# Kernel tuning notes

Hardware: AMD Instinct MI355X
Metric: run time of the kernel (lower is better)

Reference implementation:

```python
import jax, jax.numpy as jnp
import numpy as np

NUM_QUANTIZERS = 4  # num_quantizers


def setup_inputs() -> dict:
    key = jax.random.key(0)
    k1, k2 = jax.random.split(key)
    x = jax.random.normal(k1, (8, 64, 128, 128), dtype=jnp.float32)
    codebook = jax.random.normal(k2, (512, 64), dtype=jnp.float32)
    return {"x": x, "codebook": codebook}


def reference(x, codebook):
    """Residual VQ with shared Euclidean codebook, straight-through estimator.

    x: [B, C, H, W] image feature map; codebook: [K, C].
    Returns (quantized [B,C,H,W], indices [B,H,W,Q] int32, commit_loss [Q]).
    """
    B, C, H, W = x.shape
    flat = x.transpose(0, 2, 3, 1).reshape(-1, C)  # [N, C], N = B*H*W
    c_sq = jnp.sum(codebook * codebook, axis=-1)   # [K]

    residual = flat
    quant_out = jnp.zeros_like(flat)
    idx_list, losses = [], []
    for _ in range(NUM_QUANTIZERS):
        # argmin ||r - c||^2 == argmin (||c||^2 - 2 r.c); ||r||^2 constant per row
        dist = c_sq[None, :] - 2.0 * (residual @ codebook.T)  # [N, K]
        idx = jnp.argmin(dist, axis=-1)                        # [N]
        quant = codebook[idx]                                  # [N, C] gather
        # commitment loss: mse(stop_grad(quant), residual)
        losses.append(jnp.mean(jnp.square(jax.lax.stop_gradient(quant) - residual)))
        # straight-through: gradients flow to residual, not codebook
        quant_st = residual + jax.lax.stop_gradient(quant - residual)
        quant_out = quant_out + quant_st
        residual = residual - jax.lax.stop_gradient(quant)
        idx_list.append(idx)

    quantized = quant_out.reshape(B, H, W, C).transpose(0, 3, 1, 2)
    indices = jnp.stack(idx_list, axis=-1).reshape(B, H, W, NUM_QUANTIZERS)
    commit_loss = jnp.stack(losses)
    return quantized, indices, commit_loss
```

## Files before the change

kernel.cpp:

```cpp
#include <hip/hip_runtime.h>


#define NPTS   131072
#define CH     64
#define KCODE  512
#define NQ     4
#define HW     16384
#define BPTS   64
#define BTHR   256
#define CCH    8
#define NCHK   8

__device__ __forceinline__ void load_lds16(const float* g, float* l) {
    __builtin_amdgcn_global_load_lds(
        (const __attribute__((address_space(1))) void*)g,
        (__attribute__((address_space(3))) void*)l, 16, 0, 0);
}

__global__ void prep_cbS(const float* __restrict__ cb, float* __restrict__ cbS) {
    int g = blockIdx.x * 256 + threadIdx.x;
    int c = g >> 9, pos = g & 511;
    int i = pos >> 7, cg = (pos >> 2) & 31, j = pos & 3;
    int k = cg * 16 + i * 4 + j;
    cbS[g] = cb[k * CH + c];
}

__global__ void prep_csq(const float* __restrict__ cb, float* __restrict__ csq) {
    int k = blockIdx.x * 256 + threadIdx.x;
    if (k < KCODE) {
        const float4* row = (const float4*)(cb + (size_t)k * CH);
        float a0 = 0.f, a1 = 0.f, a2 = 0.f, a3 = 0.f;
#pragma unroll
        for (int j = 0; j < CH / 4; ++j) {
            float4 v = row[j];
            a0 = fmaf(v.x, v.x, a0); a1 = fmaf(v.y, v.y, a1);
            a2 = fmaf(v.z, v.z, a2); a3 = fmaf(v.w, v.w, a3);
        }
        csq[k] = (a0 + a1) + (a2 + a3);
    }
}

__global__ __launch_bounds__(BTHR, 3) void rvq_main(
    const float* __restrict__ x, const float* __restrict__ cb,
    const float* __restrict__ cbS, const float* __restrict__ csq_g,
    float* __restrict__ out_quant, float* __restrict__ out_idx,
    float* __restrict__ out_loss)
{
    __shared__ __align__(16) float s_res[CH * BPTS];
    __shared__ __align__(16) float s_buf[2][CCH * KCODE];
    __shared__ __align__(16) float s_csq[KCODE];
    __shared__ int   s_bidx[BPTS];
    __shared__ int   s_idx4[BPTS * NQ];
    __shared__ float s_ls[4 * BPTS];

    const int tid  = threadIdx.x;
    const int lane = tid & 63;
    const int w    = tid >> 6;
    const int cg   = tid & 31;
    const int pg   = tid >> 5;

    const int n0  = blockIdx.x * BPTS;
    const int b   = n0 >> 14;
    const int hw0 = n0 & (HW - 1);
    const float* xbase = x + (size_t)b * CH * HW + hw0;

#pragma unroll
    for (int r = 0; r < 4; ++r) {
        int off = (w * 4 + r) * 256;
        load_lds16(cbS + off + lane * 4, &s_buf[0][off]);
    }

    for (int j = tid; j < CH * BPTS / 4; j += BTHR) {
        int c = j >> 4, p4 = j & 15;
        *(float4*)&s_res[c * BPTS + p4 * 4] =
            *(const float4*)(xbase + (size_t)c * HW + p4 * 4);
    }
    for (int j = tid; j < KCODE; j += BTHR) s_csq[j] = csq_g[j];
    __syncthreads();

    float lossq[NQ], idxf[NQ];

    for (int q = 0; q < NQ; ++q) {
        float acc[8][16];
        {
            const float4* cq4 = (const float4*)(s_csq + cg * 16);
            float4 c0 = cq4[0], c1 = cq4[1], c2 = cq4[2], c3 = cq4[3];
            float ci[16] = {c0.x, c0.y, c0.z, c0.w, c1.x, c1.y, c1.z, c1.w,
                            c2.x, c2.y, c2.z, c2.w, c3.x, c3.y, c3.z, c3.w};
#pragma unroll
            for (int p = 0; p < 8; ++p)
#pragma unroll
                for (int n = 0; n < 16; ++n) acc[p][n] = -0.5f * ci[n];
        }

        for (int chk = 0; chk < NCHK; ++chk) {
            if (!(q == NQ - 1 && chk == NCHK - 1)) {
                const int nchk = (chk + 1 < NCHK) ? chk + 1 : 0;
                const float* src = cbS + nchk * (CCH * KCODE);
                float* dst = s_buf[(chk + 1) & 1];
#pragma unroll
                for (int r = 0; r < 4; ++r) {
                    int off = (w * 4 + r) * 256;
                    load_lds16(src + off + lane * 4, dst + off);
                }
            }

            const float* bufp = s_buf[chk & 1];
#pragma unroll 2
            for (int c = 0; c < CCH; ++c) {
                const float* ar = &s_res[(chk * CCH + c) * BPTS + pg * 8];
                float4 a0 = *(const float4*)(ar + 0);
                float4 a1 = *(const float4*)(ar + 4);
                float av[8] = {a0.x, a0.y, a0.z, a0.w, a1.x, a1.y, a1.z, a1.w};
                const float* br = &bufp[c * KCODE + cg * 4];
#pragma unroll
                for (int nb = 0; nb < 4; ++nb) {
                    float4 bq = *(const float4*)(br + nb * 128);
#pragma unroll
                    for (int p = 0; p < 8; ++p) {
                        acc[p][nb * 4 + 0] = fmaf(av[p], bq.x, acc[p][nb * 4 + 0]);
                        acc[p][nb * 4 + 1] = fmaf(av[p], bq.y, acc[p][nb * 4 + 1]);
                        acc[p][nb * 4 + 2] = fmaf(av[p], bq.z, acc[p][nb * 4 + 2]);
                        acc[p][nb * 4 + 3] = fmaf(av[p], bq.w, acc[p][nb * 4 + 3]);
                    }
                }
            }
            __syncthreads();
        }

        float bd[8]; int bi[8];
#pragma unroll
        for (int p = 0; p < 8; ++p) {
            float B = acc[p][0]; int I = cg * 16;
#pragma unroll
            for (int n = 1; n < 16; ++n)
                if (acc[p][n] > B) { B = acc[p][n]; I = cg * 16 + n; }
            bd[p] = B; bi[p] = I;
        }

#pragma unroll
        for (int m = 1; m <= 16; m <<= 1) {
#pragma unroll
            for (int p = 0; p < 8; ++p) {
                float oB = __shfl_xor(bd[p], m, 64);
                int   oI = __shfl_xor(bi[p], m, 64);
                if (oB > bd[p] || (oB == bd[p] && oI < bi[p])) {
                    bd[p] = oB; bi[p] = oI;
                }
            }
        }
        if (cg == 0) {
#pragma unroll
            for (int p = 0; p < 8; ++p) {
                s_bidx[pg * 8 + p] = bi[p];
                s_idx4[(pg * 8 + p) * 4 + q] = bi[p];
            }
        }
        __syncthreads();
        if (tid < BPTS) idxf[q] = (float)s_bidx[tid];

        {
            const int p  = tid & 63;
            const int cq = tid >> 6;
            int bix = s_bidx[p];
            const float4* crow = (const float4*)(cb + (size_t)bix * CH + cq * 16);
            float l0 = 0.f, l1 = 0.f, l2 = 0.f, l3 = 0.f;
#pragma unroll
            for (int i = 0; i < 4; ++i) {
                float4 v = crow[i];
                int c = cq * 16 + i * 4;
                float r0 = s_res[(c + 0) * BPTS + p] - v.x;
                float r1 = s_res[(c + 1) * BPTS + p] - v.y;
                float r2 = s_res[(c + 2) * BPTS + p] - v.z;
                float r3 = s_res[(c + 3) * BPTS + p] - v.w;
                s_res[(c + 0) * BPTS + p] = r0;
                s_res[(c + 1) * BPTS + p] = r1;
                s_res[(c + 2) * BPTS + p] = r2;
                s_res[(c + 3) * BPTS + p] = r3;
                l0 = fmaf(r0, r0, l0); l1 = fmaf(r1, r1, l1);
                l2 = fmaf(r2, r2, l2); l3 = fmaf(r3, r3, l3);
            }
            s_ls[cq * BPTS + p] = (l0 + l1) + (l2 + l3);
        }
        __syncthreads();
        if (tid < BPTS)
            lossq[q] = (s_ls[0 * BPTS + tid] + s_ls[1 * BPTS + tid]) +
                       (s_ls[2 * BPTS + tid] + s_ls[3 * BPTS + tid]);
    }

    {
        const int p  = tid & 63;
        const int cq = tid >> 6;
        int e0 = s_idx4[p * 4 + 0], e1 = s_idx4[p * 4 + 1];
        int e2 = s_idx4[p * 4 + 2], e3 = s_idx4[p * 4 + 3];
        const float4* r0 = (const float4*)(cb + (size_t)e0 * CH + cq * 16);
        const float4* r1 = (const float4*)(cb + (size_t)e1 * CH + cq * 16);
        const float4* r2 = (const float4*)(cb + (size_t)e2 * CH + cq * 16);
        const float4* r3 = (const float4*)(cb + (size_t)e3 * CH + cq * 16);
        float* ob = out_quant + (size_t)b * CH * HW + hw0;
#pragma unroll
        for (int i = 0; i < 4; ++i) {
            float4 v0 = r0[i], v1 = r1[i], v2 = r2[i], v3 = r3[i];
            float s0 = ((v0.x + v1.x) + v2.x) + v3.x;
            float s1 = ((v0.y + v1.y) + v2.y) + v3.y;
            float s2 = ((v0.z + v1.z) + v2.z) + v3.z;
            float s3 = ((v0.w + v1.w) + v2.w) + v3.w;
            int c = cq * 16 + i * 4;
            ob[(size_t)(c + 0) * HW + p] = s0;
            ob[(size_t)(c + 1) * HW + p] = s1;
            ob[(size_t)(c + 2) * HW + p] = s2;
            ob[(size_t)(c + 3) * HW + p] = s3;
        }
    }

    if (tid < BPTS) {
        ((float4*)out_idx)[n0 + tid] =
            make_float4(idxf[0], idxf[1], idxf[2], idxf[3]);
#pragma unroll
        for (int qq = 0; qq < NQ; ++qq) {
            float v = lossq[qq];
            for (int off = 32; off > 0; off >>= 1) v += __shfl_down(v, off, 64);
            if (tid == 0)
                atomicAdd(&out_loss[qq], v * (1.0f / 8388608.0f));
        }
    }
}

extern "C" void kernel_launch(void* const* d_in, const int* in_sizes, int n_in,
                              void* d_out, int out_size, void* d_ws, size_t ws_size,
                              hipStream_t stream) {
    const float* x  = (const float*)d_in[0];
    const float* cb = (const float*)d_in[1];
    float* out       = (float*)d_out;
    float* out_quant = out;
    float* out_idx   = out + 8388608;
    float* out_loss  = out + 8388608 + 524288;

    float* cbS = (float*)d_ws;
    float* csq = cbS + CH * KCODE;

    hipMemsetAsync(out_loss, 0, NQ * sizeof(float), stream);
    prep_cbS<<<(CH * KCODE) / 256, 256, 0, stream>>>(cb, cbS);
    prep_csq<<<2, 256, 0, stream>>>(cb, csq);
    rvq_main<<<NPTS / BPTS, BTHR, 0, stream>>>(x, cb, cbS, csq,
                                               out_quant, out_idx, out_loss);
}
```

Baseline: 521.1 us.

## Update residual scores via codebook Gram matrix with exact fallback for near ties

```diff
diff --git a/kernel.cpp b/kernel.cpp
--- a/kernel.cpp
+++ b/kernel.cpp
@@ -10,6 +10,7 @@
 #define BTHR   256
 #define CCH    8
 #define NCHK   8
+#define TAU    1.0e-2f
 
 __device__ __forceinline__ void load_lds16(const float* g, float* l) {
     __builtin_amdgcn_global_load_lds(
@@ -40,9 +41,29 @@
     }
 }
 
-__global__ __launch_bounds__(BTHR, 3) void rvq_main(
+__global__ void prep_gram(const float* __restrict__ cb, float* __restrict__ G) {
+    __shared__ float srow[CH];
+    const int kb = blockIdx.x;
+    if (threadIdx.x < CH / 4)
+        ((float4*)srow)[threadIdx.x] =
+            ((const float4*)(cb + (size_t)kb * CH))[threadIdx.x];
+    __syncthreads();
+#pragma unroll
+    for (int r = 0; r < 2; ++r) {
+        int k = threadIdx.x + r * 256;
+        const float* row = cb + (size_t)k * CH;
+        double a = 0.0;
+        for (int j = 0; j < CH; ++j) a += (double)srow[j] * (double)row[j];
+        G[(size_t)kb * KCODE + k] = (float)a;
+    }
+}
+
+__global__ __launch_bounds__(BTHR)
+__attribute__((amdgpu_waves_per_eu(3, 3)))
+void rvq_main(
     const float* __restrict__ x, const float* __restrict__ cb,
     const float* __restrict__ cbS, const float* __restrict__ csq_g,
+    const float* __restrict__ G,
     float* __restrict__ out_quant, float* __restrict__ out_idx,
     float* __restrict__ out_loss)
 {
@@ -52,6 +73,9 @@
     __shared__ int   s_bidx[BPTS];
     __shared__ int   s_idx4[BPTS * NQ];
     __shared__ float s_ls[4 * BPTS];
+    __shared__ unsigned int s_mask[2];
+    __shared__ float s_rwB[4];
+    __shared__ int   s_rwI[4];
 
     const int tid  = threadIdx.x;
     const int lane = tid & 63;
@@ -69,7 +93,6 @@
         int off = (w * 4 + r) * 256;
         load_lds16(cbS + off + lane * 4, &s_buf[0][off]);
     }
-
     for (int j = tid; j < CH * BPTS / 4; j += BTHR) {
         int c = j >> 4, p4 = j & 15;
         *(float4*)&s_res[c * BPTS + p4 * 4] =
@@ -80,83 +103,186 @@
 
     float lossq[NQ], idxf[NQ];
 
-    for (int q = 0; q < NQ; ++q) {
-        float acc[8][16];
-        {
-            const float4* cq4 = (const float4*)(s_csq + cg * 16);
-            float4 c0 = cq4[0], c1 = cq4[1], c2 = cq4[2], c3 = cq4[3];
-            float ci[16] = {c0.x, c0.y, c0.z, c0.w, c1.x, c1.y, c1.z, c1.w,
-                            c2.x, c2.y, c2.z, c2.w, c3.x, c3.y, c3.z, c3.w};
-#pragma unroll
-            for (int p = 0; p < 8; ++p)
-#pragma unroll
-                for (int n = 0; n < 16; ++n) acc[p][n] = -0.5f * ci[n];
-        }
-
-        for (int chk = 0; chk < NCHK; ++chk) {
-            if (!(q == NQ - 1 && chk == NCHK - 1)) {
-                const int nchk = (chk + 1 < NCHK) ? chk + 1 : 0;
-                const float* src = cbS + nchk * (CCH * KCODE);
-                float* dst = s_buf[(chk + 1) & 1];
-#pragma unroll
-                for (int r = 0; r < 4; ++r) {
-                    int off = (w * 4 + r) * 256;
-                    load_lds16(src + off + lane * 4, dst + off);
+    float acc[8][16];
+    {
+        const float4* cq4 = (const float4*)(s_csq + cg * 16);
+        float4 c0 = cq4[0], c1 = cq4[1], c2 = cq4[2], c3 = cq4[3];
+        float ci[16] = {c0.x, c0.y, c0.z, c0.w, c1.x, c1.y, c1.z, c1.w,
+                        c2.x, c2.y, c2.z, c2.w, c3.x, c3.y, c3.z, c3.w};
+#pragma unroll
+        for (int p = 0; p < 8; ++p)
+#pragma unroll
+            for (int n = 0; n < 16; ++n) acc[p][n] = -0.5f * ci[n];
+    }
+
+    for (int chk = 0; chk < NCHK; ++chk) {
+        if (chk < NCHK - 1) {
+            const float* src = cbS + (chk + 1) * (CCH * KCODE);
+            float* dst = s_buf[(chk + 1) & 1];
+#pragma unroll
+            for (int r = 0; r < 4; ++r) {
+                int off = (w * 4 + r) * 256;
+                load_lds16(src + off + lane * 4, dst + off);
+            }
+        }
+        const float* bufp = s_buf[chk & 1];
+#pragma unroll 2
+        for (int c = 0; c < CCH; ++c) {
+            const float* ar = &s_res[(chk * CCH + c) * BPTS + pg * 8];
+            float4 a0 = *(const float4*)(ar + 0);
+            float4 a1 = *(const float4*)(ar + 4);
+            float av[8] = {a0.x, a0.y, a0.z, a0.w, a1.x, a1.y, a1.z, a1.w};
+            const float* br = &bufp[c * KCODE + cg * 4];
+#pragma unroll
+            for (int nb = 0; nb < 4; ++nb) {
+                float4 bq = *(const float4*)(br + nb * 128);
+#pragma unroll
+                for (int p = 0; p < 8; ++p) {
+                    acc[p][nb * 4 + 0] = fmaf(av[p], bq.x, acc[p][nb * 4 + 0]);
+                    acc[p][nb * 4 + 1] = fmaf(av[p], bq.y, acc[p][nb * 4 + 1]);
+                    acc[p][nb * 4 + 2] = fmaf(av[p], bq.z, acc[p][nb * 4 + 2]);
+                    acc[p][nb * 4 + 3] = fmaf(av[p], bq.w, acc[p][nb * 4 + 3]);
                 }
             }
-
-            const float* bufp = s_buf[chk & 1];
-#pragma unroll 2
-            for (int c = 0; c < CCH; ++c) {
-                const float* ar = &s_res[(chk * CCH + c) * BPTS + pg * 8];
-                float4 a0 = *(const float4*)(ar + 0);
-                float4 a1 = *(const float4*)(ar + 4);
-                float av[8] = {a0.x, a0.y, a0.z, a0.w, a1.x, a1.y, a1.z, a1.w};
-                const float* br = &bufp[c * KCODE + cg * 4];
-#pragma unroll
-                for (int nb = 0; nb < 4; ++nb) {
-                    float4 bq = *(const float4*)(br + nb * 128);
-#pragma unroll
-                    for (int p = 0; p < 8; ++p) {
-                        acc[p][nb * 4 + 0] = fmaf(av[p], bq.x, acc[p][nb * 4 + 0]);
-                        acc[p][nb * 4 + 1] = fmaf(av[p], bq.y, acc[p][nb * 4 + 1]);
-                        acc[p][nb * 4 + 2] = fmaf(av[p], bq.z, acc[p][nb * 4 + 2]);
-                        acc[p][nb * 4 + 3] = fmaf(av[p], bq.w, acc[p][nb * 4 + 3]);
-                    }
+        }
+        __syncthreads();
+    }
+
+#pragma unroll
+    for (int p = 0; p < 8; ++p) {
+        float B = acc[p][0]; int I = cg * 16;
+#pragma unroll
+        for (int n = 1; n < 16; ++n)
+            if (acc[p][n] > B) { B = acc[p][n]; I = cg * 16 + n; }
+#pragma unroll
+        for (int m = 1; m <= 16; m <<= 1) {
+            float oB = __shfl_xor(B, m, 64);
+            int   oI = __shfl_xor(I, m, 64);
+            if (oB > B || (oB == B && oI < I)) { B = oB; I = oI; }
+        }
+        if (cg == 0) {
+            s_bidx[pg * 8 + p] = I;
+            s_idx4[(pg * 8 + p) * 4 + 0] = I;
+        }
+    }
+    __syncthreads();
+    if (tid < BPTS) idxf[0] = (float)s_bidx[tid];
+
+    {
+        const int p  = tid & 63;
+        const int cq = tid >> 6;
+        int bix = s_bidx[p];
+        const float4* crow = (const float4*)(cb + (size_t)bix * CH + cq * 16);
+        float l0 = 0.f, l1 = 0.f, l2 = 0.f, l3 = 0.f;
+#pragma unroll
+        for (int i = 0; i < 4; ++i) {
+            float4 v = crow[i];
+            int c = cq * 16 + i * 4;
+            float r0 = s_res[(c + 0) * BPTS + p] - v.x;
+            float r1 = s_res[(c + 1) * BPTS + p] - v.y;
+            float r2 = s_res[(c + 2) * BPTS + p] - v.z;
+            float r3 = s_res[(c + 3) * BPTS + p] - v.w;
+            s_res[(c + 0) * BPTS + p] = r0;
+            s_res[(c + 1) * BPTS + p] = r1;
+            s_res[(c + 2) * BPTS + p] = r2;
+            s_res[(c + 3) * BPTS + p] = r3;
+            l0 = fmaf(r0, r0, l0); l1 = fmaf(r1, r1, l1);
+            l2 = fmaf(r2, r2, l2); l3 = fmaf(r3, r3, l3);
+        }
+        s_ls[cq * BPTS + p] = (l0 + l1) + (l2 + l3);
+    }
+    __syncthreads();
+    if (tid < BPTS)
+        lossq[0] = (s_ls[0 * BPTS + tid] + s_ls[1 * BPTS + tid]) +
+                   (s_ls[2 * BPTS + tid] + s_ls[3 * BPTS + tid]);
+
+    for (int q = 1; q < NQ; ++q) {
+        int bix8[8];
+#pragma unroll
+        for (int p = 0; p < 8; ++p) bix8[p] = s_bidx[pg * 8 + p];
+        if (tid < 2) s_mask[tid] = 0;
+        __syncthreads();
+
+#pragma unroll
+        for (int p = 0; p < 8; ++p) {
+            const float4* grow =
+                (const float4*)(G + (size_t)bix8[p] * KCODE + cg * 16);
+#pragma unroll
+            for (int nb = 0; nb < 4; ++nb) {
+                float4 g = grow[nb];
+                acc[p][nb * 4 + 0] -= g.x;
+                acc[p][nb * 4 + 1] -= g.y;
+                acc[p][nb * 4 + 2] -= g.z;
+                acc[p][nb * 4 + 3] -= g.w;
+            }
+            float B = acc[p][0]; int I = cg * 16; float B2 = -3.4e38f;
+#pragma unroll
+            for (int n = 1; n < 16; ++n) {
+                float v = acc[p][n];
+                if (v > B)      { B2 = B; B = v; I = cg * 16 + n; }
+                else if (v > B2) B2 = v;
+            }
+#pragma unroll
+            for (int m = 1; m <= 16; m <<= 1) {
+                float oB  = __shfl_xor(B, m, 64);
+                int   oI  = __shfl_xor(I, m, 64);
+                float oB2 = __shfl_xor(B2, m, 64);
+                float nB2;
+                if (oB > B)       { nB2 = fmaxf(B, oB2); B = oB; I = oI; }
+                else if (oB == B) { nB2 = fmaxf(B2, oB2); if (oI < I) I = oI; }
+                else              { nB2 = fmaxf(B2, oB); }
+                B2 = nB2;
+            }
+            if (cg == 0) {
+                s_bidx[pg * 8 + p] = I;
+                s_idx4[(pg * 8 + p) * 4 + q] = I;
+                if (B - B2 < TAU)
+                    atomicOr(&s_mask[(pg * 8 + p) >> 5],
+                             1u << ((pg * 8 + p) & 31));
+            }
+        }
+        __syncthreads();
+
+        unsigned long long mask =
+            (unsigned long long)s_mask[0] |
+            ((unsigned long long)s_mask[1] << 32);
+        while (mask) {
+            int p = (int)__builtin_ctzll(mask);
+            mask &= mask - 1;
+            float Bb = -3.4e38f; int Ib = 0;
+#pragma unroll
+            for (int rr = 0; rr < 2; ++rr) {
+                int k = tid + rr * 256;
+                const float4* crow = (const float4*)(cb + (size_t)k * CH);
+                float d0 = 0.f, d1 = 0.f, d2 = 0.f, d3 = 0.f;
+#pragma unroll
+                for (int j = 0; j < 16; ++j) {
+                    float4 v = crow[j];
+                    d0 = fmaf(v.x, s_res[(j * 4 + 0) * BPTS + p], d0);
+                    d1 = fmaf(v.y, s_res[(j * 4 + 1) * BPTS + p], d1);
+                    d2 = fmaf(v.z, s_res[(j * 4 + 2) * BPTS + p], d2);
+                    d3 = fmaf(v.w, s_res[(j * 4 + 3) * BPTS + p], d3);
                 }
-            }
+                float s = fmaf(-0.5f, s_csq[k], (d0 + d1) + (d2 + d3));
+                if (s > Bb) { Bb = s; Ib = k; }
+            }
+#pragma unroll
+            for (int m = 1; m <= 32; m <<= 1) {
+                float oB = __shfl_xor(Bb, m, 64);
+                int   oI = __shfl_xor(Ib, m, 64);
+                if (oB > Bb || (oB == Bb && oI < Ib)) { Bb = oB; Ib = oI; }
+            }
+            if (lane == 0) { s_rwB[w] = Bb; s_rwI[w] = Ib; }
             __syncthreads();
-        }
-
-        float bd[8]; int bi[8];
-#pragma unroll
-        for (int p = 0; p < 8; ++p) {
-            float B = acc[p][0]; int I = cg * 16;
-#pragma unroll
-            for (int n = 1; n < 16; ++n)
-                if (acc[p][n] > B) { B = acc[p][n]; I = cg * 16 + n; }
-            bd[p] = B; bi[p] = I;
-        }
-
-#pragma unroll
-        for (int m = 1; m <= 16; m <<= 1) {
-#pragma unroll
-            for (int p = 0; p < 8; ++p) {
-                float oB = __shfl_xor(bd[p], m, 64);
-                int   oI = __shfl_xor(bi[p], m, 64);
-                if (oB > bd[p] || (oB == bd[p] && oI < bi[p])) {
-                    bd[p] = oB; bi[p] = oI;
-                }
-            }
-        }
-        if (cg == 0) {
-#pragma unroll
-            for (int p = 0; p < 8; ++p) {
-                s_bidx[pg * 8 + p] = bi[p];
-                s_idx4[(pg * 8 + p) * 4 + q] = bi[p];
-            }
-        }
-        __syncthreads();
+            float fB = s_rwB[0]; int fI = s_rwI[0];
+#pragma unroll
+            for (int ww = 1; ww < 4; ++ww) {
+                float tB = s_rwB[ww]; int tI = s_rwI[ww];
+                if (tB > fB || (tB == fB && tI < fI)) { fB = tB; fI = tI; }
+            }
+            if (tid == 0) { s_bidx[p] = fI; s_idx4[p * 4 + q] = fI; }
+            __syncthreads();
+        }
         if (tid < BPTS) idxf[q] = (float)s_bidx[tid];
 
         {
@@ -236,12 +362,14 @@
     float* out_idx   = out + 8388608;
     float* out_loss  = out + 8388608 + 524288;
 
-    float* cbS = (float*)d_ws;
+    float* G   = (float*)d_ws;
+    float* cbS = G + KCODE * KCODE;
     float* csq = cbS + CH * KCODE;
 
     hipMemsetAsync(out_loss, 0, NQ * sizeof(float), stream);
     prep_cbS<<<(CH * KCODE) / 256, 256, 0, stream>>>(cb, cbS);
     prep_csq<<<2, 256, 0, stream>>>(cb, csq);
-    rvq_main<<<NPTS / BPTS, BTHR, 0, stream>>>(x, cb, cbS, csq,
+    prep_gram<<<KCODE, 256, 0, stream>>>(cb, G);
+    rvq_main<<<NPTS / BPTS, BTHR, 0, stream>>>(x, cb, cbS, csq, G,
                                                out_quant, out_idx, out_loss);
 }
```

New measurement: 770.4 us. 47.8% more time.
